# Kernel optimization log

Hardware: AMD Instinct MI355X
Metric: run time of the kernel (lower is better)

## Reference

```python
import jax, jax.numpy as jnp
import numpy as np

N, E, G = 40000, 400000, 40
DIN, DH, DOUT = 128, 256, 128
NEG_SLOPE = 0.2  # PyG GATConv default leaky_relu slope


def _gat_layer(h_in, src, dst, W, a_src, a_dst, b, num_nodes):
    # h_in: [N, din]; src/dst: [E'] (self loops included); W: [din, dout]
    h = h_in @ W                                   # [N, dout]
    al_s = h @ a_src                               # [N]
    al_d = h @ a_dst                               # [N]
    e = jax.nn.leaky_relu(al_s[src] + al_d[dst], NEG_SLOPE)  # [E']
    # scatter-softmax over incoming edges of each dst node (stable)
    m = jax.ops.segment_max(e, dst, num_segments=num_nodes)
    ex = jnp.exp(e - m[dst])
    denom = jax.ops.segment_sum(ex, dst, num_segments=num_nodes)
    alpha = ex / denom[dst]                        # [E']
    out = jax.ops.segment_sum(h[src] * alpha[:, None], dst, num_segments=num_nodes)
    return out + b


def setup_inputs() -> dict:
    key = jax.random.key(0)
    ks = jax.random.split(key, 16)
    x = jax.random.normal(ks[0], (N, DIN), dtype=jnp.float32)
    edge_index = jax.random.randint(ks[1], (2, E), 0, N, dtype=jnp.int64)

    def lin(k, din, dout):
        return jax.random.normal(k, (din, dout), dtype=jnp.float32) / np.sqrt(din)

    def vec(k, d):
        return jax.random.normal(k, (d,), dtype=jnp.float32) / np.sqrt(d)

    return dict(
        x=x, edge_index=edge_index, num_graphs=G,
        W1=lin(ks[2], DIN, DH), a_src1=vec(ks[3], DH), a_dst1=vec(ks[4], DH), b1=jnp.zeros((DH,), jnp.float32),
        W2=lin(ks[5], DH, DH), a_src2=vec(ks[6], DH), a_dst2=vec(ks[7], DH), b2=jnp.zeros((DH,), jnp.float32),
        W3=lin(ks[8], DH, DOUT), a_src3=vec(ks[9], DOUT), a_dst3=vec(ks[10], DOUT), b3=jnp.zeros((DOUT,), jnp.float32),
    )


def reference(x, edge_index, num_graphs, W1, a_src1, a_dst1, b1, W2, a_src2, a_dst2, b2, W3, a_src3, a_dst3, b3):
    num_nodes = x.shape[0]
    # PyG GATConv adds self-loops by default
    loop = jnp.arange(num_nodes, dtype=edge_index.dtype)
    src = jnp.concatenate([edge_index[0], loop])
    dst = jnp.concatenate([edge_index[1], loop])

    h = jax.nn.relu(_gat_layer(x, src, dst, W1, a_src1, a_dst1, b1, num_nodes))
    # dropout is identity in eval mode
    h = jax.nn.relu(_gat_layer(h, src, dst, W2, a_src2, a_dst2, b2, num_nodes))
    h = _gat_layer(h, src, dst, W3, a_src3, a_dst3, b3, num_nodes)
    return h.reshape(num_graphs, num_nodes // num_graphs, -1)
```

## Files before the change

### kernel.cpp

```cpp
#include <hip/hip_runtime.h>
#include <hip/hip_bf16.h>
#include <type_traits>

typedef __attribute__((ext_vector_type(8))) short short8;
typedef __attribute__((ext_vector_type(4))) float f32x4;
typedef __attribute__((ext_vector_type(2))) float f32x2;
typedef __attribute__((ext_vector_type(8))) unsigned short u16x8;

static __device__ __forceinline__ unsigned short f2b(float f) {
    unsigned int v = __float_as_uint(f);
    unsigned int r = (v + 0x7FFFu + ((v >> 16) & 1u)) >> 16;
    return (unsigned short)r;
}
static __device__ __forceinline__ float b2f(unsigned short u) {
    return __uint_as_float(((unsigned int)u) << 16);
}

__global__ void k_init_cnt(int* cnt, int* cursor, int n) {
    int i = blockIdx.x * 256 + threadIdx.x;
    if (i < n) cnt[i] = 1;
    if (i == 0) *cursor = 0;
}

__global__ void k_hist(const int* __restrict__ dst, int* __restrict__ cnt, int E) {
    int e = blockIdx.x * 256 + threadIdx.x;
    if (e < E) atomicAdd(&cnt[dst[e]], 1);
}

__global__ void k_assign(const int* __restrict__ cnt, int* __restrict__ begptr,
                         int* __restrict__ colidx, int* __restrict__ fill,
                         int* __restrict__ cursor, int n) {
    int i = blockIdx.x * 256 + threadIdx.x;
    int lane = threadIdx.x & 63;
    int c = (i < n) ? cnt[i] : 0;
    int s = c;
#pragma unroll
    for (int off = 1; off < 64; off <<= 1) {
        int v = __shfl_up(s, off);
        if (lane >= off) s += v;
    }
    int wavesum = __shfl(s, 63);
    int base = 0;
    if (lane == 63) base = atomicAdd(cursor, wavesum);
    base = __shfl(base, 63);
    int beg = base + s - c;
    if (i < n) { begptr[i] = beg; colidx[beg] = i; fill[i] = 1; }
}

__global__ void k_scatter(const int* __restrict__ src, const int* __restrict__ dst,
                          const int* __restrict__ begptr, int* __restrict__ fill,
                          int* __restrict__ colidx, int E) {
    int e = blockIdx.x * 256 + threadIdx.x;
    if (e < E) {
        int s = src[e], d = dst[e];
        int pos = atomicAdd(&fill[d], 1);
        colidx[begptr[d] + pos] = s;
    }
}

__global__ void k_transpose(const float* __restrict__ w, unsigned short* __restrict__ wt,
                            int K, int Nc) {
    int i = blockIdx.x * 256 + threadIdx.x;
    if (i < K * Nc) {
        int k = i / Nc, n = i % Nc;
        wt[n * K + k] = f2b(w[i]);
    }
}

template<int NC, typename AT>
__global__ __launch_bounds__(256) void k_gemm(const AT* __restrict__ A,
                                              const unsigned short* __restrict__ Bt,
                                              unsigned short* __restrict__ H,
                                              const float* __restrict__ asrc,
                                              const float* __restrict__ adst,
                                              float* __restrict__ als,
                                              float* __restrict__ ald,
                                              int K) {
    __shared__ unsigned short As[64][40];
    __shared__ unsigned short Bs[NC][40];
    const int tid  = threadIdx.x;
    const int lane = tid & 63;
    const int wv   = tid >> 6;
    const int rowBase = blockIdx.x * 64;
    const int quad = lane >> 4;
    const int l16  = lane & 15;
    constexpr int NT = NC / 16;
    f32x4 acc[NT] = {};

    const int ar = tid >> 2;
    const int ak = (tid & 3) * 8;

    for (int kk = 0; kk < K; kk += 32) {
        if constexpr (std::is_same_v<AT, float>) {
            const float* ap = A + (size_t)(rowBase + ar) * K + kk + ak;
            f32x4 a0 = *(const f32x4*)ap;
            f32x4 a1 = *(const f32x4*)(ap + 4);
            short8 s;
#pragma unroll
            for (int v = 0; v < 4; v++) { s[v] = (short)f2b(a0[v]); s[4 + v] = (short)f2b(a1[v]); }
            *(short8*)&As[ar][ak] = s;
        } else {
            *(short8*)&As[ar][ak] = *(const short8*)(A + (size_t)(rowBase + ar) * K + kk + ak);
        }
#pragma unroll
        for (int c = tid; c < NC * 4; c += 256) {
            int br = c >> 2, bk = (c & 3) * 8;
            *(short8*)&Bs[br][bk] = *(const short8*)(Bt + (size_t)br * K + kk + bk);
        }
        __syncthreads();
        short8 af = *(const short8*)&As[wv * 16 + l16][quad * 8];
#pragma unroll
        for (int nt = 0; nt < NT; nt++) {
            short8 bf = *(const short8*)&Bs[nt * 16 + l16][quad * 8];
            acc[nt] = __builtin_amdgcn_mfma_f32_16x16x32_bf16(af, bf, acc[nt], 0, 0, 0);
        }
        __syncthreads();
    }

    float avs[NT], avd[NT];
#pragma unroll
    for (int nt = 0; nt < NT; nt++) {
        int gcol = nt * 16 + l16;
        avs[nt] = asrc[gcol];
        avd[nt] = adst[gcol];
#pragma unroll
        for (int r = 0; r < 4; r++) {
            int grow = rowBase + wv * 16 + quad * 4 + r;
            H[(size_t)grow * NC + gcol] = f2b(acc[nt][r]);
        }
    }
#pragma unroll
    for (int r = 0; r < 4; r++) {
        float ps = 0.f, pd = 0.f;
#pragma unroll
        for (int nt = 0; nt < NT; nt++) { ps += acc[nt][r] * avs[nt]; pd += acc[nt][r] * avd[nt]; }
#pragma unroll
        for (int off = 8; off; off >>= 1) { ps += __shfl_xor(ps, off); pd += __shfl_xor(pd, off); }
        if (l16 == 0) {
            int grow = rowBase + wv * 16 + quad * 4 + r;
            als[grow] = ps;
            ald[grow] = pd;
        }
    }
}

template<int DOUT, bool RELU, typename OutT>
__global__ __launch_bounds__(256) void k_edge(const unsigned short* __restrict__ h,
                                              const float* __restrict__ als,
                                              const float* __restrict__ ald,
                                              const int* __restrict__ begptr,
                                              const int* __restrict__ cnt,
                                              const int* __restrict__ colidx,
                                              const float* __restrict__ bias,
                                              OutT* __restrict__ out, int N) {
    int node = blockIdx.x * 4 + (threadIdx.x >> 6);
    if (node >= N) return;
    int lane = threadIdx.x & 63;
    int beg = begptr[node];
    int deg = cnt[node];
    float aldi = ald[node];

    float m = -1e30f;
    float e_lane = -1e30f;
    int   s_lane = 0;
    for (int j = lane; j < deg; j += 64) {
        int s = colidx[beg + j];
        float e = als[s] + aldi;
        e = e > 0.f ? e : 0.2f * e;
        if (j < 64) { e_lane = e; s_lane = s; }
        m = fmaxf(m, e);
    }
#pragma unroll
    for (int off = 32; off; off >>= 1) m = fmaxf(m, __shfl_xor(m, off));

    float dsum = (lane < deg) ? __expf(e_lane - m) : 0.f;
    for (int j = lane + 64; j < deg; j += 64) {
        int s = colidx[beg + j];
        float e = als[s] + aldi;
        e = e > 0.f ? e : 0.2f * e;
        dsum += __expf(e - m);
    }
#pragma unroll
    for (int off = 32; off; off >>= 1) dsum += __shfl_xor(dsum, off);
    float inv = 1.0f / dsum;
    float w_lane = (lane < deg) ? __expf(e_lane - m) * inv : 0.f;

    constexpr int QV  = DOUT / 16;
    constexpr int NC8 = QV / 8;
    const int l16g    = lane & 15;
    const int quarter = lane >> 4;
    const size_t dimOff = (size_t)l16g * QV;
    float acc[QV] = {};
    int lim = deg < 64 ? deg : 64;
    for (int t = 0; 4 * t < lim; t++) {
        int idx = 4 * t + quarter;
        float wj = __shfl(w_lane, idx);
        int   sj = __shfl(s_lane, idx);
        const unsigned short* hp = h + (size_t)sj * DOUT + dimOff;
        u16x8 c[NC8];
#pragma unroll
        for (int u = 0; u < NC8; u++) c[u] = *(const u16x8*)(hp + 8 * u);
#pragma unroll
        for (int u = 0; u < NC8; u++)
#pragma unroll
            for (int v = 0; v < 8; v++) acc[8 * u + v] += wj * b2f(c[u][v]);
    }
    for (int j = 64; j < deg; j++) {
        int sj = colidx[beg + j];
        float e = als[sj] + aldi;
        e = e > 0.f ? e : 0.2f * e;
        float wj = __expf(e - m) * inv;
        if (quarter == 0) {
            const unsigned short* hp = h + (size_t)sj * DOUT + dimOff;
#pragma unroll
            for (int u = 0; u < NC8; u++) {
                u16x8 c = *(const u16x8*)(hp + 8 * u);
#pragma unroll
                for (int v = 0; v < 8; v++) acc[8 * u + v] += wj * b2f(c[v]);
            }
        }
    }
#pragma unroll
    for (int v = 0; v < QV; v++) {
        acc[v] += __shfl_xor(acc[v], 16);
        acc[v] += __shfl_xor(acc[v], 32);
    }

    if (quarter == 0) {
        if constexpr (std::is_same_v<OutT, float>) {
            float* op = out + (size_t)node * DOUT + dimOff;
#pragma unroll
            for (int u = 0; u < QV / 4; u++) {
                f32x4 bv = *(const f32x4*)(bias + dimOff + 4 * u);
                f32x4 ov;
#pragma unroll
                for (int v = 0; v < 4; v++) {
                    float val = acc[4 * u + v] + bv[v];
                    if (RELU) val = fmaxf(val, 0.f);
                    ov[v] = val;
                }
                *(f32x4*)(op + 4 * u) = ov;
            }
        } else {
            unsigned short* op = out + (size_t)node * DOUT + dimOff;
#pragma unroll
            for (int u = 0; u < NC8; u++) {
                u16x8 ov;
#pragma unroll
                for (int v = 0; v < 8; v++) {
                    float val = acc[8 * u + v] + bias[dimOff + 8 * u + v];
                    if (RELU) val = fmaxf(val, 0.f);
                    ov[v] = f2b(val);
                }
                *(u16x8*)(op + 8 * u) = ov;
            }
        }
    }
}

extern "C" void kernel_launch(void* const* d_in, const int* in_sizes, int n_in,
                              void* d_out, int out_size, void* d_ws, size_t ws_size,
                              hipStream_t stream) {
    const int DIN = 128, DH = 256, DOUT = 128;
    const int N = in_sizes[0] / DIN;
    const int E = in_sizes[1] / 2;

    const float* x   = (const float*)d_in[0];
    const int*   ei  = (const int*)d_in[1];
    const float* W1  = (const float*)d_in[3];
    const float* as1 = (const float*)d_in[4];
    const float* ad1 = (const float*)d_in[5];
    const float* b1  = (const float*)d_in[6];
    const float* W2  = (const float*)d_in[7];
    const float* as2 = (const float*)d_in[8];
    const float* ad2 = (const float*)d_in[9];
    const float* b2  = (const float*)d_in[10];
    const float* W3  = (const float*)d_in[11];
    const float* as3 = (const float*)d_in[12];
    const float* ad3 = (const float*)d_in[13];
    const float* b3  = (const float*)d_in[14];
    float* outp = (float*)d_out;

    char* ws = (char*)d_ws;
    size_t off = 0;
    auto carve = [&](size_t bytes) { char* p = ws + off; off = (off + bytes + 255) & ~(size_t)255; return p; };
    unsigned short* hbuf = (unsigned short*)carve((size_t)N * DH * 2);
    unsigned short* gbuf = (unsigned short*)carve((size_t)N * DH * 2);
    float* als  = (float*)carve((size_t)N * 4);
    float* ald  = (float*)carve((size_t)N * 4);
    unsigned short* wt = (unsigned short*)carve((size_t)DH * DH * 2);
    int* cnt    = (int*)carve((size_t)N * 4);
    int* begptr = (int*)carve((size_t)N * 4);
    int* fill   = (int*)carve((size_t)N * 4);
    int* cursor = (int*)carve(256);
    int* colidx = (int*)carve((size_t)(E + N) * 4);
    (void)ws_size; (void)n_in; (void)out_size;

    const int* e_src = ei;
    const int* e_dst = ei + E;

    k_init_cnt<<<(N + 255) / 256, 256, 0, stream>>>(cnt, cursor, N);
    k_hist<<<(E + 255) / 256, 256, 0, stream>>>(e_dst, cnt, E);
    k_assign<<<(N + 255) / 256, 256, 0, stream>>>(cnt, begptr, colidx, fill, cursor, N);
    k_scatter<<<(E + 255) / 256, 256, 0, stream>>>(e_src, e_dst, begptr, fill, colidx, E);

    const int nblk4 = (N + 3) / 4;
    const int mblk  = N / 64;

    k_transpose<<<(DIN * DH + 255) / 256, 256, 0, stream>>>(W1, wt, DIN, DH);
    k_gemm<256, float><<<mblk, 256, 0, stream>>>(x, wt, hbuf, as1, ad1, als, ald, DIN);
    k_edge<256, true, unsigned short><<<nblk4, 256, 0, stream>>>(hbuf, als, ald, begptr, cnt, colidx, b1, gbuf, N);

    k_transpose<<<(DH * DH + 255) / 256, 256, 0, stream>>>(W2, wt, DH, DH);
    k_gemm<256, unsigned short><<<mblk, 256, 0, stream>>>(gbuf, wt, hbuf, as2, ad2, als, ald, DH);
    k_edge<256, true, unsigned short><<<nblk4, 256, 0, stream>>>(hbuf, als, ald, begptr, cnt, colidx, b2, gbuf, N);

    k_transpose<<<(DH * DOUT + 255) / 256, 256, 0, stream>>>(W3, wt, DH, DOUT);
    k_gemm<128, unsigned short><<<mblk, 256, 0, stream>>>(gbuf, wt, hbuf, as3, ad3, als, ald, DH);
    k_edge<128, false, float><<<nblk4, 256, 0, stream>>>(hbuf, als, ald, begptr, cnt, colidx, b3, outp, N);
}
```

Measured before the change: 302.5 us.

## Retile GEMM warps 2x2, merge weight transposes, replace init kernel with memset

The GEMM now gives each wave a 32-row by NC/2-column tile instead of 16 rows by all columns. Each B fragment feeds two MFMAs, which raises register-level reuse, and the per-row attention dot products are combined through shared-memory atomics. The three weight transposes are fused into one launch with separate buffers, and the count-init kernel becomes a hipMemsetAsync. The self-loop +1 is folded into k_assign and k_edge, so there are fewer launches. The cost is extra LDS atomics and another barrier in the GEMM epilogue.

```diff
diff --git a/kernel.cpp b/kernel.cpp
--- a/kernel.cpp
+++ b/kernel.cpp
@@ -4,7 +4,6 @@
 
 typedef __attribute__((ext_vector_type(8))) short short8;
 typedef __attribute__((ext_vector_type(4))) float f32x4;
-typedef __attribute__((ext_vector_type(2))) float f32x2;
 typedef __attribute__((ext_vector_type(8))) unsigned short u16x8;
 
 static __device__ __forceinline__ unsigned short f2b(float f) {
@@ -14,12 +13,6 @@
 }
 static __device__ __forceinline__ float b2f(unsigned short u) {
     return __uint_as_float(((unsigned int)u) << 16);
-}
-
-__global__ void k_init_cnt(int* cnt, int* cursor, int n) {
-    int i = blockIdx.x * 256 + threadIdx.x;
-    if (i < n) cnt[i] = 1;
-    if (i == 0) *cursor = 0;
 }
 
 __global__ void k_hist(const int* __restrict__ dst, int* __restrict__ cnt, int E) {
@@ -32,7 +25,7 @@
                          int* __restrict__ cursor, int n) {
     int i = blockIdx.x * 256 + threadIdx.x;
     int lane = threadIdx.x & 63;
-    int c = (i < n) ? cnt[i] : 0;
+    int c = (i < n) ? cnt[i] + 1 : 0;
     int s = c;
 #pragma unroll
     for (int off = 1; off < 64; off <<= 1) {
@@ -58,12 +51,21 @@
     }
 }
 
-__global__ void k_transpose(const float* __restrict__ w, unsigned short* __restrict__ wt,
-                            int K, int Nc) {
+__global__ void k_transpose3(const float* __restrict__ w1, unsigned short* __restrict__ t1,
+                             const float* __restrict__ w2, unsigned short* __restrict__ t2,
+                             const float* __restrict__ w3, unsigned short* __restrict__ t3,
+                             int K1, int N1, int K2, int N2, int K3, int N3) {
     int i = blockIdx.x * 256 + threadIdx.x;
-    if (i < K * Nc) {
-        int k = i / Nc, n = i % Nc;
-        wt[n * K + k] = f2b(w[i]);
+    int n1 = K1 * N1, n2 = K2 * N2, n3 = K3 * N3;
+    if (i < n1) {
+        int k = i / N1, n = i % N1;
+        t1[n * K1 + k] = f2b(w1[i]);
+    } else if (i < n1 + n2) {
+        int j = i - n1, k = j / N2, n = j % N2;
+        t2[n * K2 + k] = f2b(w2[j]);
+    } else if (i < n1 + n2 + n3) {
+        int j = i - n1 - n2, k = j / N3, n = j % N3;
+        t3[n * K3 + k] = f2b(w3[j]);
     }
 }
 
@@ -78,14 +80,19 @@
                                               int K) {
     __shared__ unsigned short As[64][40];
     __shared__ unsigned short Bs[NC][40];
+    __shared__ float sps[64], spd[64];
     const int tid  = threadIdx.x;
     const int lane = tid & 63;
     const int wv   = tid >> 6;
     const int rowBase = blockIdx.x * 64;
     const int quad = lane >> 4;
     const int l16  = lane & 15;
-    constexpr int NT = NC / 16;
-    f32x4 acc[NT] = {};
+    constexpr int CG = NC / 32;
+    const int wrow = (wv & 1) * 32;
+    const int wcol = (wv >> 1) * (NC / 2);
+    f32x4 acc[2][CG] = {};
+
+    if (tid < 64) { sps[tid] = 0.f; spd[tid] = 0.f; }
 
     const int ar = tid >> 2;
     const int ak = (tid & 3) * 8;
@@ -108,40 +115,48 @@
             *(short8*)&Bs[br][bk] = *(const short8*)(Bt + (size_t)br * K + kk + bk);
         }
         __syncthreads();
-        short8 af = *(const short8*)&As[wv * 16 + l16][quad * 8];
-#pragma unroll
-        for (int nt = 0; nt < NT; nt++) {
-            short8 bf = *(const short8*)&Bs[nt * 16 + l16][quad * 8];
-            acc[nt] = __builtin_amdgcn_mfma_f32_16x16x32_bf16(af, bf, acc[nt], 0, 0, 0);
+        short8 af0 = *(const short8*)&As[wrow + l16][quad * 8];
+        short8 af1 = *(const short8*)&As[wrow + 16 + l16][quad * 8];
+#pragma unroll
+        for (int cg = 0; cg < CG; cg++) {
+            short8 bf = *(const short8*)&Bs[wcol + cg * 16 + l16][quad * 8];
+            acc[0][cg] = __builtin_amdgcn_mfma_f32_16x16x32_bf16(af0, bf, acc[0][cg], 0, 0, 0);
+            acc[1][cg] = __builtin_amdgcn_mfma_f32_16x16x32_bf16(af1, bf, acc[1][cg], 0, 0, 0);
         }
         __syncthreads();
     }
 
-    float avs[NT], avd[NT];
-#pragma unroll
-    for (int nt = 0; nt < NT; nt++) {
-        int gcol = nt * 16 + l16;
-        avs[nt] = asrc[gcol];
-        avd[nt] = adst[gcol];
+    float avs[CG], avd[CG];
+#pragma unroll
+    for (int cg = 0; cg < CG; cg++) {
+        int gcol = wcol + cg * 16 + l16;
+        avs[cg] = asrc[gcol];
+        avd[cg] = adst[gcol];
+#pragma unroll
+        for (int rg = 0; rg < 2; rg++)
+#pragma unroll
+            for (int r = 0; r < 4; r++) {
+                int grow = rowBase + wrow + rg * 16 + quad * 4 + r;
+                H[(size_t)grow * NC + gcol] = f2b(acc[rg][cg][r]);
+            }
+    }
+#pragma unroll
+    for (int rg = 0; rg < 2; rg++)
 #pragma unroll
         for (int r = 0; r < 4; r++) {
-            int grow = rowBase + wv * 16 + quad * 4 + r;
-            H[(size_t)grow * NC + gcol] = f2b(acc[nt][r]);
-        }
-    }
-#pragma unroll
-    for (int r = 0; r < 4; r++) {
-        float ps = 0.f, pd = 0.f;
-#pragma unroll
-        for (int nt = 0; nt < NT; nt++) { ps += acc[nt][r] * avs[nt]; pd += acc[nt][r] * avd[nt]; }
-#pragma unroll
-        for (int off = 8; off; off >>= 1) { ps += __shfl_xor(ps, off); pd += __shfl_xor(pd, off); }
-        if (l16 == 0) {
-            int grow = rowBase + wv * 16 + quad * 4 + r;
-            als[grow] = ps;
-            ald[grow] = pd;
-        }
-    }
+            float ps = 0.f, pd = 0.f;
+#pragma unroll
+            for (int cg = 0; cg < CG; cg++) { ps += acc[rg][cg][r] * avs[cg]; pd += acc[rg][cg][r] * avd[cg]; }
+#pragma unroll
+            for (int off = 8; off; off >>= 1) { ps += __shfl_xor(ps, off); pd += __shfl_xor(pd, off); }
+            if (l16 == 0) {
+                int lrow = wrow + rg * 16 + quad * 4 + r;
+                atomicAdd(&sps[lrow], ps);
+                atomicAdd(&spd[lrow], pd);
+            }
+        }
+    __syncthreads();
+    if (tid < 64) { als[rowBase + tid] = sps[tid]; ald[rowBase + tid] = spd[tid]; }
 }
 
 template<int DOUT, bool RELU, typename OutT>
@@ -157,7 +172,8 @@
     if (node >= N) return;
     int lane = threadIdx.x & 63;
     int beg = begptr[node];
-    int deg = cnt[node];
+    int deg = cnt[node] + 1;
+
     float aldi = ald[node];
 
     float m = -1e30f;
@@ -288,18 +304,27 @@
     unsigned short* gbuf = (unsigned short*)carve((size_t)N * DH * 2);
     float* als  = (float*)carve((size_t)N * 4);
     float* ald  = (float*)carve((size_t)N * 4);
-    unsigned short* wt = (unsigned short*)carve((size_t)DH * DH * 2);
+    unsigned short* wt1 = (unsigned short*)carve((size_t)DIN * DH * 2);
+    unsigned short* wt2 = (unsigned short*)carve((size_t)DH * DH * 2);
+    unsigned short* wt3 = (unsigned short*)carve((size_t)DH * DOUT * 2);
     int* cnt    = (int*)carve((size_t)N * 4);
+    int* cursor = (int*)carve(256);
     int* begptr = (int*)carve((size_t)N * 4);
     int* fill   = (int*)carve((size_t)N * 4);
-    int* cursor = (int*)carve(256);
     int* colidx = (int*)carve((size_t)(E + N) * 4);
     (void)ws_size; (void)n_in; (void)out_size;
 
     const int* e_src = ei;
     const int* e_dst = ei + E;
 
-    k_init_cnt<<<(N + 255) / 256, 256, 0, stream>>>(cnt, cursor, N);
+    hipMemsetAsync(cnt, 0, (size_t)((char*)cursor - (char*)cnt) + 4, stream);
+
+    {
+        int tot = DIN * DH + DH * DH + DH * DOUT;
+        k_transpose3<<<(tot + 255) / 256, 256, 0, stream>>>(W1, wt1, W2, wt2, W3, wt3,
+                                                            DIN, DH, DH, DH, DH, DOUT);
+    }
+
     k_hist<<<(E + 255) / 256, 256, 0, stream>>>(e_dst, cnt, E);
     k_assign<<<(N + 255) / 256, 256, 0, stream>>>(cnt, begptr, colidx, fill, cursor, N);
     k_scatter<<<(E + 255) / 256, 256, 0, stream>>>(e_src, e_dst, begptr, fill, colidx, E);
@@ -307,15 +332,12 @@
     const int nblk4 = (N + 3) / 4;
     const int mblk  = N / 64;
 
-    k_transpose<<<(DIN * DH + 255) / 256, 256, 0, stream>>>(W1, wt, DIN, DH);
-    k_gemm<256, float><<<mblk, 256, 0, stream>>>(x, wt, hbuf, as1, ad1, als, ald, DIN);
+    k_gemm<256, float><<<mblk, 256, 0, stream>>>(x, wt1, hbuf, as1, ad1, als, ald, DIN);
     k_edge<256, true, unsigned short><<<nblk4, 256, 0, stream>>>(hbuf, als, ald, begptr, cnt, colidx, b1, gbuf, N);
 
-    k_transpose<<<(DH * DH + 255) / 256, 256, 0, stream>>>(W2, wt, DH, DH);
-    k_gemm<256, unsigned short><<<mblk, 256, 0, stream>>>(gbuf, wt, hbuf, as2, ad2, als, ald, DH);
+    k_gemm<256, unsigned short><<<mblk, 256, 0, stream>>>(gbuf, wt2, hbuf, as2, ad2, als, ald, DH);
     k_edge<256, true, unsigned short><<<nblk4, 256, 0, stream>>>(hbuf, als, ald, begptr, cnt, colidx, b2, gbuf, N);
 
-    k_transpose<<<(DH * DOUT + 255) / 256, 256, 0, stream>>>(W3, wt, DH, DOUT);
-    k_gemm<128, unsigned short><<<mblk, 256, 0, stream>>>(gbuf, wt, hbuf, as3, ad3, als, ald, DH);
+    k_gemm<128, unsigned short><<<mblk, 256, 0, stream>>>(gbuf, wt3, hbuf, as3, ad3, als, ald, DH);
     k_edge<128, false, float><<<nblk4, 256, 0, stream>>>(hbuf, als, ald, begptr, cnt, colidx, b3, outp, N);
 }
```

New measurement: 301.9 us. No clear change (-0.2%).
